# Kernel optimization log

Measured on AMD Instinct MI355X. Metric: run time of the kernel, lower is better.

Reference implementation:

```python
import jax, jax.numpy as jnp
import numpy as np

B, N, C, H = 4, 1024, 1024, 16
D = C // H  # head_dim = 64


def setup_inputs() -> dict:
    key = jax.random.key(0)
    k1, k2, k3 = jax.random.split(key, 3)
    x = jax.random.normal(k1, (B, N, C), dtype=jnp.float32)
    Wqkv = jax.random.normal(k2, (3 * C, C), dtype=jnp.float32) * (C ** -0.5)
    Wproj = jax.random.normal(k3, (C, C), dtype=jnp.float32) * (C ** -0.5)
    bproj = jnp.zeros((C,), dtype=jnp.float32)
    epoch = 25  # selects mask_2 (window w=8) per the original branching
    return {"x": x, "Wqkv": Wqkv, "Wproj": Wproj, "bproj": bproj, "epoch": epoch}


def _band_mask(n, w):
    # get_attn_mask(N, w) == (|i - j| <= w) for every row (boundary cases included)
    idx = jnp.arange(n)
    return jnp.abs(idx[:, None] - idx[None, :]) <= w


def reference(x, Wqkv, Wproj, bproj, epoch):
    b, n, c = x.shape
    d = c // H
    # qkv linear (no bias), then the module's per-head interleaved split:
    # view(B,N,H,3d) -> permute(B,H,N,3d) -> tensor_split into q,k,v
    qkv = jnp.einsum('bnc,oc->bno', x, Wqkv)            # [B,N,3C]
    qkv = qkv.reshape(b, n, H, 3 * d).transpose(0, 2, 1, 3)  # [B,H,N,3d]
    q, k, v = jnp.split(qkv, 3, axis=-1)                # each [B,H,N,d]
    scale = d ** -0.5
    score = jnp.einsum('bhid,bhjd->bhij', q, k) * scale  # [B,H,N,N]
    if epoch is not None and epoch < 50:
        if epoch < 20:
            w = 6
        elif epoch < 30:
            w = 8
        elif epoch < 40:
            w = 10
        else:
            w = 12
        mask = _band_mask(n, w)  # [N,N] bool
        score = jnp.where(mask[None, None], score, jnp.float32(-1e9))
    attn = jax.nn.softmax(score, axis=-1)
    ctx = jnp.einsum('bhij,bhjd->bhid', attn, v)         # [B,H,N,d]
    ctx = ctx.transpose(0, 2, 1, 3).reshape(b, n, c)     # [B,N,C]
    out = jnp.einsum('bnc,oc->bno', ctx, Wproj) + bproj
    return out
```

## Files before the change

kernel.cpp:

```cpp
#include <hip/hip_runtime.h>
#include <hip/hip_bf16.h>


typedef __bf16 bf16x8_t __attribute__((ext_vector_type(8)));
typedef unsigned short u16x8_t __attribute__((ext_vector_type(8)));
typedef float f32x4_t __attribute__((ext_vector_type(4)));

__device__ __forceinline__ void load_lds16(const void* g, void* l) {
    __builtin_amdgcn_global_load_lds(
        (__attribute__((address_space(1))) void*)(g),
        (__attribute__((address_space(3))) void*)(l),
        16, 0, 0);
}

__global__ __launch_bounds__(256) void convert_all(
    const float* __restrict__ x, const float* __restrict__ wqkv,
    const float* __restrict__ wproj,
    __hip_bfloat16* __restrict__ xb, __hip_bfloat16* __restrict__ wqkvb,
    __hip_bfloat16* __restrict__ wprojb)
{
    const size_t t = (size_t)blockIdx.x * 256 + threadIdx.x;
    size_t i = t * 8;
    const float* src;
    __hip_bfloat16* dst;
    if (i < 4194304) {
        src = x; dst = xb;
    } else if (i < 4194304 + 3145728) {
        src = wqkv; dst = wqkvb; i -= 4194304;
    } else {
        src = wproj; dst = wprojb; i -= 4194304 + 3145728;
    }
    float4 v0 = *reinterpret_cast<const float4*>(src + i);
    float4 v1 = *reinterpret_cast<const float4*>(src + i + 4);
    union { u16x8_t v; __hip_bfloat16 h[8]; } u;
    u.h[0] = __float2bfloat16(v0.x); u.h[1] = __float2bfloat16(v0.y);
    u.h[2] = __float2bfloat16(v0.z); u.h[3] = __float2bfloat16(v0.w);
    u.h[4] = __float2bfloat16(v1.x); u.h[5] = __float2bfloat16(v1.y);
    u.h[6] = __float2bfloat16(v1.z); u.h[7] = __float2bfloat16(v1.w);
    *reinterpret_cast<u16x8_t*>(dst + i) = u.v;
}

__global__ __launch_bounds__(512, 2) void gemm1_qkv256(
    const __hip_bfloat16* __restrict__ A,
    const __hip_bfloat16* __restrict__ B,
    __hip_bfloat16* __restrict__ C)
{
    __shared__ __align__(16) char smem[114688];
    const int tid = threadIdx.x;

    const int orig = blockIdx.y * 16 + blockIdx.x;
    const int xcd = orig & 7, slot = orig >> 3;
    const int hi = slot >> 4;
    const int s  = xcd * 2 + hi;
    const int w  = slot & 15;
    const int m0 = ((s & 3) * 4 + (w & 3)) * 256;
    const int n0 = ((s >> 2) * 4 + (w >> 2)) * 192;

    const int wave = tid >> 6, lane = tid & 63;
    const int wr = wave >> 2, wc = wave & 3;
    const int lr = lane & 15, kg = lane >> 4;
    const int K = 1024, Nn = 3072;

    const int qa0 = tid, qa1 = tid + 512;
    const int qb0 = tid, qb1 = tid + 256;
    const int ra0 = qa0 >> 2, sa0 = ((qa0 & 3) ^ ((ra0 >> 1) & 3)) * 16;
    const int ra1 = qa1 >> 2, sa1 = ((qa1 & 3) ^ ((ra1 >> 1) & 3)) * 16;
    const int rb0 = qb0 >> 2, sb0 = ((qb0 & 3) ^ ((rb0 >> 1) & 3)) * 16;
    const int rb1 = qb1 >> 2, sb1 = ((qb1 & 3) ^ ((rb1 >> 1) & 3)) * 16;
    const char* Asrc0 = (const char*)(A + (size_t)(m0 + ra0) * K) + sa0;
    const char* Asrc1 = (const char*)(A + (size_t)(m0 + ra1) * K) + sa1;
    const char* Bsrc0 = (const char*)(B + (size_t)(n0 + rb0) * K) + sb0;
    const char* Bsrc1 = (const char*)(B + (size_t)(n0 + rb1) * K) + sb1;
    const bool bextra = (tid >= 256);

#define STAGE1(t) { const int sb_ = ((t) & 3) * 28672; const int ko_ = (t) * 64;  \
    load_lds16(Asrc0 + ko_, smem + sb_ + qa0 * 16);                                \
    load_lds16(Asrc1 + ko_, smem + sb_ + qa1 * 16);                                \
    load_lds16(Bsrc0 + ko_, smem + sb_ + 16384 + qb0 * 16);                        \
    if (bextra) load_lds16(Bsrc1 + ko_, smem + sb_ + 16384 + qb1 * 16); }

    f32x4_t acc[8][3] = {};
    const int rsw = ((kg ^ ((lr >> 1) & 3)) * 16);
    const int arow = wr * 128 + lr;
    const int brow = wc * 48 + lr;

#define COMPUTE1(t) { const int sb_ = ((t) & 3) * 28672;                           \
    bf16x8_t a_[8], b_[3];                                                         \
    _Pragma("unroll") for (int mi = 0; mi < 8; ++mi)                               \
        a_[mi] = *(const bf16x8_t*)(smem + sb_ + (arow + mi * 16) * 64 + rsw);     \
    _Pragma("unroll") for (int ni = 0; ni < 3; ++ni)                               \
        b_[ni] = *(const bf16x8_t*)(smem + sb_ + 16384 + (brow + ni * 16) * 64 + rsw); \
    __builtin_amdgcn_s_setprio(1);                                                 \
    _Pragma("unroll") for (int mi = 0; mi < 8; ++mi)                               \
    _Pragma("unroll") for (int ni = 0; ni < 3; ++ni)                               \
        acc[mi][ni] = __builtin_amdgcn_mfma_f32_16x16x32_bf16(                     \
            a_[mi], b_[ni], acc[mi][ni], 0, 0, 0);                                 \
    __builtin_amdgcn_s_setprio(0); }

    STAGE1(0);
    STAGE1(1);
    for (int t = 0; t < 30; ++t) {
        STAGE1(t + 2);
        asm volatile("s_waitcnt vmcnt(6)" ::: "memory");
        __builtin_amdgcn_s_barrier();
        COMPUTE1(t);
    }
    asm volatile("s_waitcnt vmcnt(3)" ::: "memory");
    __builtin_amdgcn_s_barrier();
    COMPUTE1(30);
    asm volatile("s_waitcnt vmcnt(0)" ::: "memory");
    __builtin_amdgcn_s_barrier();
    COMPUTE1(31);
#undef STAGE1
#undef COMPUTE1

    __syncthreads();
    __hip_bfloat16* cl = (__hip_bfloat16*)smem;
#pragma unroll
    for (int mi = 0; mi < 8; ++mi)
#pragma unroll
        for (int ni = 0; ni < 3; ++ni)
#pragma unroll
            for (int r = 0; r < 4; ++r)
                cl[(wr * 128 + mi * 16 + kg * 4 + r) * 200 + wc * 48 + ni * 16 + lr] =
                    __float2bfloat16(acc[mi][ni][r]);
    __syncthreads();
#pragma unroll
    for (int c = 0; c < 12; ++c) {
        const int id = tid + c * 512;
        const int row = id / 24, cc = id - row * 24;
        f32x4_t v = *(const f32x4_t*)(smem + row * 400 + cc * 16);
        *(f32x4_t*)((char*)C + ((size_t)(m0 + row) * Nn + n0) * 2 + cc * 16) = v;
    }
}

__global__ __launch_bounds__(256) void gemm2_proj(
    const __hip_bfloat16* __restrict__ A,
    const __hip_bfloat16* __restrict__ B,
    float* __restrict__ C,
    const float* __restrict__ bias)
{
    __shared__ char smem[16384];
    const int tid = threadIdx.x;
    const int orig = blockIdx.y * 8 + blockIdx.x;
    const int wgid = (orig & 7) * 64 + (orig >> 3);
    const int n0 = (wgid & 7) * 128, m0 = (wgid >> 3) * 64;
    const int wave = tid >> 6, lane = tid & 63;
    const int wr = wave >> 1, wc = wave & 1;
    const int lr = lane & 15, kg = lane >> 4;
    const int K = 1024, Nn = 1024;

    f32x4_t acc[2][4] = {};

    for (int k0 = 0; k0 < K; k0 += 32) {
        __syncthreads();
        {
            const int row = tid >> 2, cb = (tid & 3) * 8;
            load_lds16(A + (size_t)(m0 + row) * K + k0 + cb, smem + tid * 16);
        }
#pragma unroll
        for (int it = 0; it < 2; ++it) {
            const int c = tid + it * 256;
            const int row = c >> 2, cb = (c & 3) * 8;
            load_lds16(B + (size_t)(n0 + row) * K + k0 + cb,
                       smem + 4096 + c * 16);
        }
        __syncthreads();

        bf16x8_t a[2], b[4];
#pragma unroll
        for (int mi = 0; mi < 2; ++mi)
            a[mi] = *reinterpret_cast<const bf16x8_t*>(
                smem + ((wr * 32 + mi * 16 + lr) * 32 + kg * 8) * 2);
#pragma unroll
        for (int ni = 0; ni < 4; ++ni)
            b[ni] = *reinterpret_cast<const bf16x8_t*>(
                smem + 4096 + ((wc * 64 + ni * 16 + lr) * 32 + kg * 8) * 2);
#pragma unroll
        for (int mi = 0; mi < 2; ++mi)
#pragma unroll
            for (int ni = 0; ni < 4; ++ni)
                acc[mi][ni] = __builtin_amdgcn_mfma_f32_16x16x32_bf16(
                    a[mi], b[ni], acc[mi][ni], 0, 0, 0);
    }

    __syncthreads();
#pragma unroll
    for (int p = 0; p < 2; ++p) {
        if (p) __syncthreads();
        if (wr == p) {
#pragma unroll
            for (int mi = 0; mi < 2; ++mi)
#pragma unroll
                for (int ni = 0; ni < 4; ++ni) {
                    const int scol = wc * 64 + ni * 16 + lr;
#pragma unroll
                    for (int r = 0; r < 4; ++r) {
                        const int srow = mi * 16 + kg * 4 + r;
                        ((float*)smem)[srow * 128 + scol] = acc[mi][ni][r];
                    }
                }
        }
        __syncthreads();
#pragma unroll
        for (int cc = 0; cc < 4; ++cc) {
            const int chunk = tid + cc * 256;
            const int srow = chunk >> 5;
            const int sc = (chunk & 31) * 4;
            f32x4_t v = *reinterpret_cast<const f32x4_t*>(smem + chunk * 16);
            const f32x4_t bv = *reinterpret_cast<const f32x4_t*>(bias + n0 + sc);
            v += bv;
            *reinterpret_cast<f32x4_t*>(
                C + (size_t)(m0 + p * 32 + srow) * Nn + n0 + sc) = v;
        }
    }
}

__global__ __launch_bounds__(256) void attn_band_mfma(
    const __hip_bfloat16* __restrict__ qkv,
    __hip_bfloat16* __restrict__ ctx,
    const int* __restrict__ epoch_ptr)
{
    __shared__ __align__(16) __hip_bfloat16 K_lds[128 * 64];
    __shared__ __align__(16) __hip_bfloat16 V_lds[64 * 136];
    __shared__ __hip_bfloat16 P_lds[4][16 * 40];

    const int tid = threadIdx.x;
    const int wave = tid >> 6, lane = tid & 63;
    const int lr = lane & 15, kg = lane >> 4;

    const int bid = blockIdx.x;
    const int tg = bid & 15;
    const int bh = bid >> 4;
    const int h = bh & 15, b = bh >> 4;
    const int base = tg * 64;
    const int i0 = base + wave * 16;

    const int e = *epoch_ptr;
    int w;
    if      (e < 20) w = 6;
    else if (e < 30) w = 8;
    else if (e < 40) w = 10;
    else if (e < 50) w = 12;
    else             w = 1023;

    const size_t rowb = (size_t)b * 1024;
    const int hq = h * 192;

#pragma unroll
    for (int it = 0; it < 4; ++it) {
        const int q = tid + it * 256;
        const int row = q >> 3, s = q & 7;
        const int c = s ^ (row & 7);
        int gk = base - 32 + row;
        gk = gk < 0 ? 0 : (gk > 1023 ? 1023 : gk);
        load_lds16(qkv + (rowb + gk) * 3072 + hq + 64 + c * 8,
                   (char*)K_lds + q * 16);
    }
    {
        const int pr = tid & 63, dg = tid >> 6;
        int gk0 = base - 32 + 2 * pr, gk1 = gk0 + 1;
        gk0 = gk0 < 0 ? 0 : (gk0 > 1023 ? 1023 : gk0);
        gk1 = gk1 < 0 ? 0 : (gk1 > 1023 ? 1023 : gk1);
        const __hip_bfloat16* v0 = qkv + (rowb + gk0) * 3072 + hq + 128 + dg * 16;
        const __hip_bfloat16* v1 = qkv + (rowb + gk1) * 3072 + hq + 128 + dg * 16;
        u16x8_t a0 = *(const u16x8_t*)v0, b0 = *(const u16x8_t*)(v0 + 8);
        u16x8_t a1 = *(const u16x8_t*)v1, b1 = *(const u16x8_t*)(v1 + 8);
#pragma unroll
        for (int c2 = 0; c2 < 8; ++c2) {
            *(unsigned int*)&V_lds[(dg * 16 + c2) * 136 + 2 * pr] =
                (unsigned int)a0[c2] | ((unsigned int)a1[c2] << 16);
            *(unsigned int*)&V_lds[(dg * 16 + 8 + c2) * 136 + 2 * pr] =
                (unsigned int)b0[c2] | ((unsigned int)b1[c2] << 16);
        }
    }

    bf16x8_t aq[2];
#pragma unroll
    for (int ks = 0; ks < 2; ++ks)
        aq[ks] = *(const bf16x8_t*)(qkv + (rowb + i0 + lr) * 3072 + hq + ks * 32 + kg * 8);

    __syncthreads();

    float m[4] = {-1e30f, -1e30f, -1e30f, -1e30f};
    float l[4] = {0.f, 0.f, 0.f, 0.f};
    f32x4_t o[4] = {};

    int jlo = i0 - w;      if (jlo < 0) jlo = 0;
    int jhi = i0 + 15 + w; if (jhi > 1023) jhi = 1023;
    const int t0 = (base >> 5) - 1;

    for (int p = (jlo >> 5); p <= (jhi >> 5); ++p) {
        const int kb = p * 32;
        const int tl = p - t0;

        f32x4_t s2[2] = {};
#pragma unroll
        for (int t = 0; t < 2; ++t)
#pragma unroll
            for (int ks = 0; ks < 2; ++ks) {
                const int lkr = tl * 32 + t * 16 + lr;
                bf16x8_t bk = *(const bf16x8_t*)(
                    (char*)K_lds + lkr * 128 + (((ks * 4 + kg) ^ (lr & 7)) * 16));
                s2[t] = __builtin_amdgcn_mfma_f32_16x16x32_bf16(aq[ks], bk, s2[t], 0, 0, 0);
            }

        float sv[2][4];
#pragma unroll
        for (int t = 0; t < 2; ++t)
#pragma unroll
            for (int r = 0; r < 4; ++r) {
                const int qi = i0 + kg * 4 + r;
                const int j  = kb + t * 16 + lr;
                int d = qi - j; if (d < 0) d = -d;
                sv[t][r] = (d <= w) ? s2[t][r] * 0.125f : -1e30f;
            }

        float tm[4];
#pragma unroll
        for (int r = 0; r < 4; ++r) tm[r] = fmaxf(sv[0][r], sv[1][r]);
#pragma unroll
        for (int msk = 1; msk < 16; msk <<= 1)
#pragma unroll
            for (int r = 0; r < 4; ++r) tm[r] = fmaxf(tm[r], __shfl_xor(tm[r], msk));

        float sc[4], ps[4], pvv[2][4];
#pragma unroll
        for (int r = 0; r < 4; ++r) {
            const float mn = fmaxf(m[r], tm[r]);
            sc[r] = __expf(m[r] - mn);
            pvv[0][r] = __expf(sv[0][r] - mn);
            pvv[1][r] = __expf(sv[1][r] - mn);
            ps[r] = pvv[0][r] + pvv[1][r];
            m[r] = mn;
        }
#pragma unroll
        for (int msk = 1; msk < 16; msk <<= 1)
#pragma unroll
            for (int r = 0; r < 4; ++r) ps[r] += __shfl_xor(ps[r], msk);
#pragma unroll
        for (int r = 0; r < 4; ++r) l[r] = l[r] * sc[r] + ps[r];
#pragma unroll
        for (int ni = 0; ni < 4; ++ni)
#pragma unroll
            for (int r = 0; r < 4; ++r) o[ni][r] *= sc[r];

#pragma unroll
        for (int t = 0; t < 2; ++t)
#pragma unroll
            for (int r = 0; r < 4; ++r)
                P_lds[wave][(kg * 4 + r) * 40 + t * 16 + lr] =
                    __float2bfloat16(pvv[t][r]);

        bf16x8_t ap = *(const bf16x8_t*)&P_lds[wave][lr * 40 + kg * 8];
#pragma unroll
        for (int ni = 0; ni < 4; ++ni) {
            bf16x8_t bv = *(const bf16x8_t*)&V_lds[(ni * 16 + lr) * 136 + tl * 32 + kg * 8];
            o[ni] = __builtin_amdgcn_mfma_f32_16x16x32_bf16(ap, bv, o[ni], 0, 0, 0);
        }
    }

#pragma unroll
    for (int ni = 0; ni < 4; ++ni)
#pragma unroll
        for (int r = 0; r < 4; ++r)
            ctx[(rowb + i0 + kg * 4 + r) * 1024 + h * 64 + ni * 16 + lr] =
                __float2bfloat16(o[ni][r] / l[r]);
}

extern "C" void kernel_launch(void* const* d_in, const int* in_sizes, int n_in,
                              void* d_out, int out_size, void* d_ws, size_t ws_size,
                              hipStream_t stream)
{
    const float* x     = (const float*)d_in[0];
    const float* Wqkv  = (const float*)d_in[1];
    const float* Wproj = (const float*)d_in[2];
    const float* bproj = (const float*)d_in[3];
    const int*   epoch = (const int*)d_in[4];

    char* ws = (char*)d_ws;
    __hip_bfloat16* xb     = (__hip_bfloat16*)(ws);
    __hip_bfloat16* wqkvb  = (__hip_bfloat16*)(ws + 8388608);
    __hip_bfloat16* wprojb = (__hip_bfloat16*)(ws + 8388608 + 6291456);
    __hip_bfloat16* qkvb   = (__hip_bfloat16*)(ws + 16777216);
    __hip_bfloat16* ctxb   = (__hip_bfloat16*)(ws + 16777216 + 25165824);

    convert_all<<<4096, 256, 0, stream>>>(x, Wqkv, Wproj, xb, wqkvb, wprojb);

    gemm1_qkv256<<<dim3(16, 16), 512, 0, stream>>>(xb, wqkvb, qkvb);

    attn_band_mfma<<<1024, 256, 0, stream>>>(qkvb, ctxb, epoch);

    gemm2_proj<<<dim3(1024 / 128, 4096 / 64), 256, 0, stream>>>(
        ctxb, wprojb, (float*)d_out, bproj);
}
```

Measured before the change: 73.63 us.

## Split QKV GEMM main loop into half-steps and rewrite projection GEMM as pipelined 128x128

The QKV GEMM loop now splits each k-step into two halves of the M tile. A and B tile loads are interleaved between the MFMA halves with extra barriers, aiming to overlap global-to-LDS traffic with compute more finely. The output projection GEMM moves from a synchronous 64x128 tile with 256 threads to a 128x128 tile with 512 threads. It uses a 4-stage swizzled LDS ring buffer with direct-to-LDS loads and waitcnt-based pipelining, so per-k-step syncs and LDS bank conflicts should drop. The costs are more barriers per step in gemm1 and larger LDS and register use in gemm2, which may limit occupancy.

Result: no change. 73.93 us (+0.4%).

```diff
diff --git a/kernel.cpp b/kernel.cpp
--- a/kernel.cpp
+++ b/kernel.cpp
@@ -73,9 +73,10 @@
     const char* Bsrc1 = (const char*)(B + (size_t)(n0 + rb1) * K) + sb1;
     const bool bextra = (tid >= 256);
 
-#define STAGE1(t) { const int sb_ = ((t) & 3) * 28672; const int ko_ = (t) * 64;  \
+#define STAGE_A(t) { const int sb_ = ((t) & 3) * 28672; const int ko_ = (t) * 64; \
     load_lds16(Asrc0 + ko_, smem + sb_ + qa0 * 16);                                \
-    load_lds16(Asrc1 + ko_, smem + sb_ + qa1 * 16);                                \
+    load_lds16(Asrc1 + ko_, smem + sb_ + qa1 * 16); }
+#define STAGE_B(t) { const int sb_ = ((t) & 3) * 28672; const int ko_ = (t) * 64; \
     load_lds16(Bsrc0 + ko_, smem + sb_ + 16384 + qb0 * 16);                        \
     if (bextra) load_lds16(Bsrc1 + ko_, smem + sb_ + 16384 + qb1 * 16); }
 
@@ -84,35 +85,55 @@
     const int arow = wr * 128 + lr;
     const int brow = wc * 48 + lr;
 
-#define COMPUTE1(t) { const int sb_ = ((t) & 3) * 28672;                           \
-    bf16x8_t a_[8], b_[3];                                                         \
-    _Pragma("unroll") for (int mi = 0; mi < 8; ++mi)                               \
-        a_[mi] = *(const bf16x8_t*)(smem + sb_ + (arow + mi * 16) * 64 + rsw);     \
-    _Pragma("unroll") for (int ni = 0; ni < 3; ++ni)                               \
-        b_[ni] = *(const bf16x8_t*)(smem + sb_ + 16384 + (brow + ni * 16) * 64 + rsw); \
-    __builtin_amdgcn_s_setprio(1);                                                 \
-    _Pragma("unroll") for (int mi = 0; mi < 8; ++mi)                               \
-    _Pragma("unroll") for (int ni = 0; ni < 3; ++ni)                               \
-        acc[mi][ni] = __builtin_amdgcn_mfma_f32_16x16x32_bf16(                     \
-            a_[mi], b_[ni], acc[mi][ni], 0, 0, 0);                                 \
-    __builtin_amdgcn_s_setprio(0); }
-
-    STAGE1(0);
-    STAGE1(1);
-    for (int t = 0; t < 30; ++t) {
-        STAGE1(t + 2);
-        asm volatile("s_waitcnt vmcnt(6)" ::: "memory");
-        __builtin_amdgcn_s_barrier();
-        COMPUTE1(t);
-    }
-    asm volatile("s_waitcnt vmcnt(3)" ::: "memory");
+    STAGE_A(0); STAGE_B(0);
+    STAGE_A(1); STAGE_B(1);
+    if (!bextra) { asm volatile("s_waitcnt vmcnt(4)" ::: "memory"); }
+    else         { asm volatile("s_waitcnt vmcnt(3)" ::: "memory"); }
     __builtin_amdgcn_s_barrier();
-    COMPUTE1(30);
-    asm volatile("s_waitcnt vmcnt(0)" ::: "memory");
-    __builtin_amdgcn_s_barrier();
-    COMPUTE1(31);
-#undef STAGE1
-#undef COMPUTE1
+
+    for (int t = 0; t < 32; ++t) {
+        const int sb_ = (t & 3) * 28672;
+        bf16x8_t a_[8], b_[3];
+#pragma unroll
+        for (int mi = 0; mi < 4; ++mi)
+            a_[mi] = *(const bf16x8_t*)(smem + sb_ + (arow + mi * 16) * 64 + rsw);
+#pragma unroll
+        for (int ni = 0; ni < 3; ++ni)
+            b_[ni] = *(const bf16x8_t*)(smem + sb_ + 16384 + (brow + ni * 16) * 64 + rsw);
+        if (t < 30) STAGE_A(t + 2);
+        __builtin_amdgcn_s_barrier();
+        __builtin_amdgcn_s_setprio(1);
+#pragma unroll
+        for (int mi = 0; mi < 4; ++mi)
+#pragma unroll
+            for (int ni = 0; ni < 3; ++ni)
+                acc[mi][ni] = __builtin_amdgcn_mfma_f32_16x16x32_bf16(
+                    a_[mi], b_[ni], acc[mi][ni], 0, 0, 0);
+        __builtin_amdgcn_s_setprio(0);
+        __builtin_amdgcn_s_barrier();
+#pragma unroll
+        for (int mi = 4; mi < 8; ++mi)
+            a_[mi] = *(const bf16x8_t*)(smem + sb_ + (arow + mi * 16) * 64 + rsw);
+        if (t < 30) {
+            STAGE_B(t + 2);
+            if (!bextra) { asm volatile("s_waitcnt vmcnt(4)" ::: "memory"); }
+            else         { asm volatile("s_waitcnt vmcnt(3)" ::: "memory"); }
+        } else {
+            asm volatile("s_waitcnt vmcnt(0)" ::: "memory");
+        }
+        __builtin_amdgcn_s_barrier();
+        __builtin_amdgcn_s_setprio(1);
+#pragma unroll
+        for (int mi = 4; mi < 8; ++mi)
+#pragma unroll
+            for (int ni = 0; ni < 3; ++ni)
+                acc[mi][ni] = __builtin_amdgcn_mfma_f32_16x16x32_bf16(
+                    a_[mi], b_[ni], acc[mi][ni], 0, 0, 0);
+        __builtin_amdgcn_s_setprio(0);
+        __builtin_amdgcn_s_barrier();
+    }
+#undef STAGE_A
+#undef STAGE_B
 
     __syncthreads();
     __hip_bfloat16* cl = (__hip_bfloat16*)smem;
@@ -134,84 +155,97 @@
     }
 }
 
-__global__ __launch_bounds__(256) void gemm2_proj(
+__global__ __launch_bounds__(512, 2) void gemm2_proj128(
     const __hip_bfloat16* __restrict__ A,
     const __hip_bfloat16* __restrict__ B,
     float* __restrict__ C,
     const float* __restrict__ bias)
 {
-    __shared__ char smem[16384];
+    __shared__ __align__(16) char smem[65536];
     const int tid = threadIdx.x;
     const int orig = blockIdx.y * 8 + blockIdx.x;
-    const int wgid = (orig & 7) * 64 + (orig >> 3);
-    const int n0 = (wgid & 7) * 128, m0 = (wgid >> 3) * 64;
+    const int wgid = (orig & 7) * 32 + (orig >> 3);
+    const int m0 = (wgid >> 3) * 128, n0 = (wgid & 7) * 128;
+
     const int wave = tid >> 6, lane = tid & 63;
-    const int wr = wave >> 1, wc = wave & 1;
+    const int wr = wave >> 2, wc = wave & 3;
     const int lr = lane & 15, kg = lane >> 4;
     const int K = 1024, Nn = 1024;
 
-    f32x4_t acc[2][4] = {};
-
-    for (int k0 = 0; k0 < K; k0 += 32) {
-        __syncthreads();
-        {
-            const int row = tid >> 2, cb = (tid & 3) * 8;
-            load_lds16(A + (size_t)(m0 + row) * K + k0 + cb, smem + tid * 16);
-        }
-#pragma unroll
-        for (int it = 0; it < 2; ++it) {
-            const int c = tid + it * 256;
-            const int row = c >> 2, cb = (c & 3) * 8;
-            load_lds16(B + (size_t)(n0 + row) * K + k0 + cb,
-                       smem + 4096 + c * 16);
-        }
-        __syncthreads();
-
-        bf16x8_t a[2], b[4];
-#pragma unroll
-        for (int mi = 0; mi < 2; ++mi)
-            a[mi] = *reinterpret_cast<const bf16x8_t*>(
-                smem + ((wr * 32 + mi * 16 + lr) * 32 + kg * 8) * 2);
-#pragma unroll
-        for (int ni = 0; ni < 4; ++ni)
-            b[ni] = *reinterpret_cast<const bf16x8_t*>(
-                smem + 4096 + ((wc * 64 + ni * 16 + lr) * 32 + kg * 8) * 2);
-#pragma unroll
-        for (int mi = 0; mi < 2; ++mi)
-#pragma unroll
-            for (int ni = 0; ni < 4; ++ni)
+    const int q = tid;
+    const int row = q >> 2, sl = ((q & 3) ^ ((row >> 1) & 3)) * 16;
+    const char* Asrc = (const char*)(A + (size_t)(m0 + row) * K) + sl;
+    const char* Bsrc = (const char*)(B + (size_t)(n0 + row) * K) + sl;
+
+#define STAGE2(t) { const int sb_ = ((t) & 3) * 16384; const int ko_ = (t) * 64; \
+    load_lds16(Asrc + ko_, smem + sb_ + q * 16);                                  \
+    load_lds16(Bsrc + ko_, smem + sb_ + 8192 + q * 16); }
+
+    f32x4_t acc[4][2] = {};
+    const int rsw = ((kg ^ ((lr >> 1) & 3)) * 16);
+    const int arow = wr * 64 + lr;
+    const int brow = wc * 32 + lr;
+
+    STAGE2(0); STAGE2(1);
+    asm volatile("s_waitcnt vmcnt(2)" ::: "memory");
+    __builtin_amdgcn_s_barrier();
+
+    for (int t = 0; t < 32; ++t) {
+        const int sb_ = (t & 3) * 16384;
+        if (t < 30) {
+            STAGE2(t + 2);
+            asm volatile("s_waitcnt vmcnt(4)" ::: "memory");
+        } else if (t == 30) {
+            asm volatile("s_waitcnt vmcnt(2)" ::: "memory");
+        } else {
+            asm volatile("s_waitcnt vmcnt(0)" ::: "memory");
+        }
+        __builtin_amdgcn_s_barrier();
+        bf16x8_t a_[4], b_[2];
+#pragma unroll
+        for (int mi = 0; mi < 4; ++mi)
+            a_[mi] = *(const bf16x8_t*)(smem + sb_ + (arow + mi * 16) * 64 + rsw);
+#pragma unroll
+        for (int ni = 0; ni < 2; ++ni)
+            b_[ni] = *(const bf16x8_t*)(smem + sb_ + 8192 + (brow + ni * 16) * 64 + rsw);
+        __builtin_amdgcn_s_setprio(1);
+#pragma unroll
+        for (int mi = 0; mi < 4; ++mi)
+#pragma unroll
+            for (int ni = 0; ni < 2; ++ni)
                 acc[mi][ni] = __builtin_amdgcn_mfma_f32_16x16x32_bf16(
-                    a[mi], b[ni], acc[mi][ni], 0, 0, 0);
-    }
+                    a_[mi], b_[ni], acc[mi][ni], 0, 0, 0);
+        __builtin_amdgcn_s_setprio(0);
+        __builtin_amdgcn_s_barrier();
+    }
+#undef STAGE2
 
     __syncthreads();
+    float* cf = (float*)smem;
 #pragma unroll
     for (int p = 0; p < 2; ++p) {
         if (p) __syncthreads();
         if (wr == p) {
 #pragma unroll
-            for (int mi = 0; mi < 2; ++mi)
-#pragma unroll
-                for (int ni = 0; ni < 4; ++ni) {
-                    const int scol = wc * 64 + ni * 16 + lr;
-#pragma unroll
-                    for (int r = 0; r < 4; ++r) {
-                        const int srow = mi * 16 + kg * 4 + r;
-                        ((float*)smem)[srow * 128 + scol] = acc[mi][ni][r];
-                    }
+            for (int mi = 0; mi < 4; ++mi)
+#pragma unroll
+                for (int ni = 0; ni < 2; ++ni) {
+                    const int scol = wc * 32 + ni * 16 + lr;
+#pragma unroll
+                    for (int r = 0; r < 4; ++r)
+                        cf[(mi * 16 + kg * 4 + r) * 132 + scol] = acc[mi][ni][r];
                 }
         }
         __syncthreads();
 #pragma unroll
         for (int cc = 0; cc < 4; ++cc) {
-            const int chunk = tid + cc * 256;
+            const int chunk = tid + cc * 512;
             const int srow = chunk >> 5;
             const int sc = (chunk & 31) * 4;
-            f32x4_t v = *reinterpret_cast<const f32x4_t*>(smem + chunk * 16);
-            const f32x4_t bv = *reinterpret_cast<const f32x4_t*>(bias + n0 + sc);
+            f32x4_t v = *(const f32x4_t*)(smem + srow * 528 + sc * 4);
+            const f32x4_t bv = *(const f32x4_t*)(bias + n0 + sc);
             v += bv;
-            *reinterpret_cast<f32x4_t*>(
-                C + (size_t)(m0 + p * 32 + srow) * Nn + n0 + sc) = v;
+            *(f32x4_t*)(C + (size_t)(m0 + p * 64 + srow) * Nn + n0 + sc) = v;
         }
     }
 }
@@ -391,6 +425,6 @@
 
     attn_band_mfma<<<1024, 256, 0, stream>>>(qkvb, ctxb, epoch);
 
-    gemm2_proj<<<dim3(1024 / 128, 4096 / 64), 256, 0, stream>>>(
+    gemm2_proj128<<<dim3(8, 32), 512, 0, stream>>>(
         ctxb, wprojb, (float*)d_out, bproj);
 }
```
